# Optimization experiments

Measured on AMD Instinct MI355X. Metric: run time of the kernel, lower is better.

The kernel has to match this reference:

```python
import jax, jax.numpy as jnp
import numpy as np


def setup_inputs() -> dict:
    key = jax.random.key(0)
    k_u, k_a, k_b, k_c, k_d = jax.random.split(key, 5)
    B, T, Din, Dout, S = 16, 4096, 256, 256, 256
    return {
        "u": jax.random.normal(k_u, (B, T, Din), dtype=jnp.float32),
        "a_raw": jnp.zeros((S,), dtype=jnp.float32),
        "b": jax.random.normal(k_b, (S, Din), dtype=jnp.float32) * 0.1,
        "c": jax.random.normal(k_c, (Dout, S), dtype=jnp.float32) * 0.1,
        "d": jax.random.normal(k_d, (Dout, Din), dtype=jnp.float32) * 0.1,
    }


def reference(u, a_raw, b, c, d):
    # u: (B, T, Din) -> y: (B, T, Dout)
    # Recurrence: x_t = a * x_{t-1} + b @ u_t ;  y_t = c @ x_t + d @ u_t
    a = jnp.tanh(a_raw)                                  # (S,)
    Bu = jnp.einsum('btd,sd->bts', u, b)                 # input projection, (B,T,S)

    def step(x, bu_t):
        x = x * a + bu_t                                 # diagonal state update
        return x, x

    x0 = jnp.zeros((u.shape[0], a.shape[0]), dtype=u.dtype)
    _, xs = jax.lax.scan(step, x0, jnp.swapaxes(Bu, 0, 1))  # xs: (T,B,S)
    xs = jnp.swapaxes(xs, 0, 1)                              # (B,T,S)

    y = jnp.einsum('bts,os->bto', xs, c) + jnp.einsum('bti,oi->bto', u, d)
    return y  # dropout(p=0.0) is identity
```

## Files before the change

### kernel.cpp

```cpp
#include <hip/hip_runtime.h>

#define DEV __device__ __forceinline__

typedef unsigned short u16;
typedef __attribute__((ext_vector_type(8))) __bf16 bf16x8;
typedef __attribute__((ext_vector_type(4))) float f32x4;
typedef __attribute__((ext_vector_type(8))) unsigned short u16x8;

static constexpr int NCH_TOT = 1024;

DEV u16 f2bf(float f) {
  unsigned u = __builtin_bit_cast(unsigned, f);
  u += 0x7fffu + ((u >> 16) & 1u);
  return (u16)(u >> 16);
}
DEV float bf2f(u16 h) {
  unsigned u = ((unsigned)h) << 16;
  return __builtin_bit_cast(float, u);
}

DEV void gl_lds16(const void* gp, void* lp) {
  __builtin_amdgcn_global_load_lds(
      (__attribute__((address_space(1))) void*)(void*)gp,
      (__attribute__((address_space(3))) void*)lp, 16, 0, 0);
}

__global__ __launch_bounds__(256) void prep_k(const float* __restrict__ a_raw,
                                              const float* __restrict__ b,
                                              const float* __restrict__ c,
                                              const float* __restrict__ d,
                                              float* __restrict__ af,
                                              u16* __restrict__ bw,
                                              u16* __restrict__ cw,
                                              u16* __restrict__ dw) {
  int i = blockIdx.x * 256 + threadIdx.x;
  if (i < 256) af[i] = tanhf(a_raw[i]);
  bw[i] = f2bf(b[i]);
  cw[i] = f2bf(c[i]);
  dw[i] = f2bf(d[i]);
}

__global__ __launch_bounds__(256) void convu_k(const float* __restrict__ u,
                                               u16* __restrict__ ub) {
  size_t i = ((size_t)blockIdx.x * 256 + threadIdx.x) * 8;
  float4 v0 = *reinterpret_cast<const float4*>(u + i);
  float4 v1 = *reinterpret_cast<const float4*>(u + i + 4);
  u16x8 o;
  o[0] = f2bf(v0.x); o[1] = f2bf(v0.y); o[2] = f2bf(v0.z); o[3] = f2bf(v0.w);
  o[4] = f2bf(v1.x); o[5] = f2bf(v1.y); o[6] = f2bf(v1.z); o[7] = f2bf(v1.w);
  *reinterpret_cast<u16x8*>(ub + i) = o;
}

__global__ __launch_bounds__(256) void gemm1_k(const u16* __restrict__ ubf,
                                               const u16* __restrict__ bw,
                                               const float* __restrict__ af,
                                               u16* __restrict__ bu,
                                               float* __restrict__ carry4) {
  __shared__ u16 As[128 * 64];
  __shared__ u16 Bs[128 * 64];
  const int tid = threadIdx.x;
  const int lane = tid & 63;
  const int wid = tid >> 6;
  const int wm = wid >> 1, wn = wid & 1;
  const int panel = blockIdx.x;
  const size_t row0 = (size_t)blockIdx.y * 128;
  const int col0 = panel * 128;

  const int rstg = tid >> 3;
  const int c16 = tid & 7;

  const f32x4 zero = {0.f, 0.f, 0.f, 0.f};
  f32x4 acc[4][4];
#pragma unroll
  for (int i = 0; i < 4; ++i)
#pragma unroll
    for (int j = 0; j < 4; ++j) acc[i][j] = zero;

#pragma unroll
  for (int kt = 0; kt < 4; ++kt) {
    const int kb = kt * 64;
#pragma unroll
    for (int j = 0; j < 4; ++j) {
      int row = j * 32 + rstg;
      int sc = c16 ^ (row & 7);
      gl_lds16(ubf + (row0 + row) * 256 + kb + sc * 8,
               (char*)As + j * 4096 + wid * 1024);
      gl_lds16(bw + (size_t)(col0 + row) * 256 + kb + sc * 8,
               (char*)Bs + j * 4096 + wid * 1024);
    }
    __syncthreads();
#pragma unroll
    for (int kk = 0; kk < 2; ++kk) {
      const int ks = kk * 4 + (lane >> 4);
      bf16x8 afr[4], bfr[4];
#pragma unroll
      for (int mi = 0; mi < 4; ++mi) {
        int ar = wm * 64 + mi * 16 + (lane & 15);
        afr[mi] = *reinterpret_cast<const bf16x8*>(&As[ar * 64 + (ks ^ (ar & 7)) * 8]);
      }
#pragma unroll
      for (int ni = 0; ni < 4; ++ni) {
        int br = wn * 64 + ni * 16 + (lane & 15);
        bfr[ni] = *reinterpret_cast<const bf16x8*>(&Bs[br * 64 + (ks ^ (br & 7)) * 8]);
      }
#pragma unroll
      for (int mi = 0; mi < 4; ++mi)
#pragma unroll
        for (int ni = 0; ni < 4; ++ni)
          acc[mi][ni] = __builtin_amdgcn_mfma_f32_16x16x32_bf16(
              afr[mi], bfr[ni], acc[mi][ni], 0, 0, 0);
    }
    if (kt < 3) __syncthreads();
  }

  const size_t t2 = (size_t)blockIdx.y * 2 + wm;
#pragma unroll
  for (int mi = 0; mi < 4; ++mi) {
    int rbase = mi * 16 + (lane >> 4) * 4;
#pragma unroll
    for (int ni = 0; ni < 4; ++ni) {
      int col = col0 + wn * 64 + ni * 16 + (lane & 15);
      int colpart = (col >> 6) * 4096 + (col & 7);
      int sl = (col >> 3) & 7;
#pragma unroll
      for (int q = 0; q < 4; ++q) {
        int r = rbase + q;
        bu[t2 * 16384 + colpart + r * 64 + ((sl ^ (r & 7)) * 8)] = f2bf(acc[mi][ni][q]);
      }
    }
  }

  {
    const int tb = (lane >> 4) * 4;
#pragma unroll
    for (int ni = 0; ni < 4; ++ni) {
      int col = col0 + wn * 64 + ni * 16 + (lane & 15);
      float a = af[col];
      float c2 = a * a, c4 = c2 * c2, c8 = c4 * c4, a12 = c8 * c4;
      float base = (tb == 0) ? a12 : (tb == 4) ? c8 : (tb == 8) ? c4 : 1.0f;
#pragma unroll
      for (int mi = 0; mi < 4; ++mi) {
        float p = base, sq = 0.f;
#pragma unroll
        for (int q = 3; q >= 0; --q) {
          sq = fmaf(p, acc[mi][ni][q], sq);
          if (q) p *= a;
        }
        sq += __shfl_xor(sq, 16, 64);
        sq += __shfl_xor(sq, 32, 64);
        if ((lane >> 4) == 0) carry4[t2 * 1024 + mi * 256 + col] = sq;
      }
    }
  }
}

__global__ __launch_bounds__(256) void scan2_k(const float* __restrict__ carry4,
                                               const float* __restrict__ af,
                                               float* __restrict__ initb4) {
  int b = blockIdx.x;
  int s = threadIdx.x;
  float a = af[s];
  float a16 = a * a; a16 = a16 * a16; a16 = a16 * a16; a16 = a16 * a16;
  float x = 0.f;
  size_t base = (size_t)b * 64 * 1024 + s;
  float c0 = carry4[base], c1 = carry4[base + 256],
        c2 = carry4[base + 512], c3 = carry4[base + 768];
  for (int k = 0; k < 64; ++k) {
    size_t idx = base + (size_t)k * 1024;
    float n0 = 0.f, n1 = 0.f, n2 = 0.f, n3 = 0.f;
    if (k < 63) {
      size_t nx = idx + 1024;
      n0 = carry4[nx]; n1 = carry4[nx + 256]; n2 = carry4[nx + 512]; n3 = carry4[nx + 768];
    }
    initb4[idx] = x;        x = fmaf(a16, x, c0);
    initb4[idx + 256] = x;  x = fmaf(a16, x, c1);
    initb4[idx + 512] = x;  x = fmaf(a16, x, c2);
    initb4[idx + 768] = x;  x = fmaf(a16, x, c3);
    c0 = n0; c1 = n1; c2 = n2; c3 = n3;
  }
}

__global__ __launch_bounds__(512, 6) void gemm2_k(const u16* __restrict__ bu,
                                                  const u16* __restrict__ cw,
                                                  const u16* __restrict__ dw,
                                                  const u16* __restrict__ ubf,
                                                  const float* __restrict__ af,
                                                  const float* __restrict__ initb4,
                                                  float* __restrict__ y) {
  __shared__ u16 XS[64 * 256];
  __shared__ u16 CS[128 * 64];
  const int tid = threadIdx.x;
  const int lane = tid & 63;
  const int wid = tid >> 6;
  const int wr = wid >> 2, wc = wid & 3;
  const int by = blockIdx.y;
  const int col0 = blockIdx.x * 128;

  const char* src = (const char*)bu + (size_t)by * 32768;
#pragma unroll
  for (int j = 0; j < 4; ++j)
    gl_lds16(src + j * 8192 + tid * 16, (char*)XS + j * 8192 + wid * 1024);
#pragma unroll
  for (int rr = 0; rr < 2; ++rr) {
    int brow = rr * 64 + (tid >> 3);
    int sc = (tid & 7) ^ (brow & 7);
    gl_lds16(cw + (size_t)(col0 + brow) * 256 + sc * 8,
             (char*)CS + rr * 8192 + wid * 1024);
  }
  __syncthreads();

  {
    const int s = tid & 255;
    const int pair = tid >> 8;
    const float a = af[s];
    const int colpart = (s >> 6) * 4096 + (s & 7);
    const int sl = (s >> 3) & 7;
    float x1 = initb4[(size_t)by * 1024 + (pair * 2) * 256 + s];
    float x2 = initb4[(size_t)by * 1024 + (pair * 2 + 1) * 256 + s];
    const int rA0 = pair * 32, rB0 = pair * 32 + 16;
    float vA[16], vB[16];
#pragma unroll
    for (int t = 0; t < 16; ++t) {
      int rA = rA0 + t, rB = rB0 + t;
      vA[t] = bf2f(XS[colpart + rA * 64 + ((sl ^ (rA & 7)) * 8)]);
      vB[t] = bf2f(XS[colpart + rB * 64 + ((sl ^ (rB & 7)) * 8)]);
    }
#pragma unroll
    for (int t = 0; t < 16; ++t) {
      x1 = fmaf(a, x1, vA[t]); vA[t] = x1;
      x2 = fmaf(a, x2, vB[t]); vB[t] = x2;
    }
#pragma unroll
    for (int t = 0; t < 16; ++t) {
      int rA = rA0 + t, rB = rB0 + t;
      XS[colpart + rA * 64 + ((sl ^ (rA & 7)) * 8)] = f2bf(vA[t]);
      XS[colpart + rB * 64 + ((sl ^ (rB & 7)) * 8)] = f2bf(vB[t]);
    }
  }
  __syncthreads();

  f32x4 acc[2][2];
  const f32x4 zero = {0.f, 0.f, 0.f, 0.f};
  acc[0][0] = zero; acc[0][1] = zero; acc[1][0] = zero; acc[1][1] = zero;

#pragma unroll
  for (int kt8 = 0; kt8 < 8; ++kt8) {
#pragma unroll
    for (int kk = 0; kk < 2; ++kk) {
      const int ksl = kk * 4 + (lane >> 4);
      bf16x8 afr[2], bfr[2];
#pragma unroll
      for (int mi = 0; mi < 2; ++mi) {
        int ar = wr * 32 + mi * 16 + (lane & 15);
        afr[mi] = *reinterpret_cast<const bf16x8*>(
            &XS[(kt8 & 3) * 4096 + ar * 64 + ((ksl ^ (ar & 7)) * 8)]);
      }
#pragma unroll
      for (int ni = 0; ni < 2; ++ni) {
        int nr = wc * 32 + ni * 16 + (lane & 15);
        bfr[ni] = *reinterpret_cast<const bf16x8*>(&CS[nr * 64 + ((ksl ^ (nr & 7)) * 8)]);
      }
#pragma unroll
      for (int mi = 0; mi < 2; ++mi)
#pragma unroll
        for (int ni = 0; ni < 2; ++ni)
          acc[mi][ni] = __builtin_amdgcn_mfma_f32_16x16x32_bf16(
              afr[mi], bfr[ni], acc[mi][ni], 0, 0, 0);
    }
    if (kt8 < 7) {
      __syncthreads();
      if (kt8 < 4) {
        int r = tid >> 3, cs = tid & 7;
        gl_lds16(ubf + ((size_t)by * 64 + r) * 256 + kt8 * 64 + ((cs ^ (r & 7)) * 8),
                 (char*)XS + kt8 * 8192 + wid * 1024);
      }
      const u16* Wn = (kt8 < 3) ? cw : dw;
      const int kb = (kt8 < 3) ? (kt8 + 1) * 64 : (kt8 - 3) * 64;
#pragma unroll
      for (int rr = 0; rr < 2; ++rr) {
        int brow = rr * 64 + (tid >> 3);
        int sc = (tid & 7) ^ (brow & 7);
        gl_lds16(Wn + (size_t)(col0 + brow) * 256 + kb + sc * 8,
                 (char*)CS + rr * 8192 + wid * 1024);
      }
      __syncthreads();
    }
  }

#pragma unroll
  for (int mi = 0; mi < 2; ++mi) {
    int rlb = wr * 32 + mi * 16 + (lane >> 4) * 4;
#pragma unroll
    for (int ni = 0; ni < 2; ++ni) {
      int col = col0 + wc * 32 + ni * 16 + (lane & 15);
#pragma unroll
      for (int q = 0; q < 4; ++q)
        y[((size_t)by * 64 + rlb + q) * 256 + col] = acc[mi][ni][q];
    }
  }
}

extern "C" void kernel_launch(void* const* d_in, const int* in_sizes, int n_in,
                              void* d_out, int out_size, void* d_ws, size_t ws_size,
                              hipStream_t stream) {
  const float* u = (const float*)d_in[0];
  const float* a_raw = (const float*)d_in[1];
  const float* b = (const float*)d_in[2];
  const float* c = (const float*)d_in[3];
  const float* d = (const float*)d_in[4];
  float* y = (float*)d_out;
  char* ws = (char*)d_ws;

  const size_t MB = 1u << 20;
  float* af = (float*)(ws);
  u16* bw = (u16*)(ws + 4096);
  u16* cw = (u16*)(ws + 4096 + 131072);
  u16* dw = (u16*)(ws + 4096 + 2 * 131072);
  u16* ubf = (u16*)(ws + 1 * MB);
  u16* bu = (u16*)(ws + 33 * MB);
  float* carry4 = (float*)(ws + 65 * MB);
  float* initb4 = (float*)(ws + 69 * MB);

  prep_k<<<256, 256, 0, stream>>>(a_raw, b, c, d, af, bw, cw, dw);
  convu_k<<<8192, 256, 0, stream>>>(u, ubf);
  gemm1_k<<<dim3(2, 512), 256, 0, stream>>>(ubf, bw, af, bu, carry4);
  scan2_k<<<16, 256, 0, stream>>>(carry4, af, initb4);
  gemm2_k<<<dim3(2, 1024), 512, 0, stream>>>(bu, cw, dw, ubf, af, initb4, y);
}
```

Measured before the change: 96.27 us.

## Double-buffer LDS tiles in both GEMM kernels to overlap loads with MFMA

gemm1 and gemm2 now keep two LDS buffers for the weight/input tiles. Each k-step issues the next tile's async global-to-LDS loads before running the MFMAs on the current tile, which removes one barrier per step and hides load latency behind compute. gemm2 also prefetches the second C tile during the in-LDS scan, and splits that scan into 8-step segments to cut register pressure. The costs are more LDS per block, a lower launch-bounds occupancy hint (6 to 4), and one redundant reload of C tile 1 on the first iteration.

After: 100.5 us. 1.04x slower.

```diff
diff --git a/kernel.cpp b/kernel.cpp
--- a/kernel.cpp
+++ b/kernel.cpp
@@ -6,8 +6,6 @@
 typedef __attribute__((ext_vector_type(8))) __bf16 bf16x8;
 typedef __attribute__((ext_vector_type(4))) float f32x4;
 typedef __attribute__((ext_vector_type(8))) unsigned short u16x8;
-
-static constexpr int NCH_TOT = 1024;
 
 DEV u16 f2bf(float f) {
   unsigned u = __builtin_bit_cast(unsigned, f);
@@ -56,8 +54,8 @@
                                                const float* __restrict__ af,
                                                u16* __restrict__ bu,
                                                float* __restrict__ carry4) {
-  __shared__ u16 As[128 * 64];
-  __shared__ u16 Bs[128 * 64];
+  __shared__ u16 As[2 * 128 * 64];
+  __shared__ u16 Bs[2 * 128 * 64];
   const int tid = threadIdx.x;
   const int lane = tid & 63;
   const int wid = tid >> 6;
@@ -76,19 +74,28 @@
 #pragma unroll
     for (int j = 0; j < 4; ++j) acc[i][j] = zero;
 
+#define G1_STAGE(ktv, bufv)                                                  \
+  {                                                                          \
+    const int kb_ = (ktv) * 64;                                              \
+    _Pragma("unroll") for (int j = 0; j < 4; ++j) {                          \
+      int row = j * 32 + rstg;                                               \
+      int sc = c16 ^ (row & 7);                                              \
+      gl_lds16(ubf + (row0 + row) * 256 + kb_ + sc * 8,                      \
+               (char*)As + (bufv)*16384 + j * 4096 + wid * 1024);            \
+      gl_lds16(bw + (size_t)(col0 + row) * 256 + kb_ + sc * 8,               \
+               (char*)Bs + (bufv)*16384 + j * 4096 + wid * 1024);            \
+    }                                                                        \
+  }
+
+  G1_STAGE(0, 0);
+  __syncthreads();
+
 #pragma unroll
   for (int kt = 0; kt < 4; ++kt) {
-    const int kb = kt * 64;
-#pragma unroll
-    for (int j = 0; j < 4; ++j) {
-      int row = j * 32 + rstg;
-      int sc = c16 ^ (row & 7);
-      gl_lds16(ubf + (row0 + row) * 256 + kb + sc * 8,
-               (char*)As + j * 4096 + wid * 1024);
-      gl_lds16(bw + (size_t)(col0 + row) * 256 + kb + sc * 8,
-               (char*)Bs + j * 4096 + wid * 1024);
-    }
-    __syncthreads();
+    const int cur = kt & 1;
+    if (kt < 3) G1_STAGE(kt + 1, cur ^ 1);
+    const u16* Ab = As + cur * 8192;
+    const u16* Bb = Bs + cur * 8192;
 #pragma unroll
     for (int kk = 0; kk < 2; ++kk) {
       const int ks = kk * 4 + (lane >> 4);
@@ -96,12 +103,12 @@
 #pragma unroll
       for (int mi = 0; mi < 4; ++mi) {
         int ar = wm * 64 + mi * 16 + (lane & 15);
-        afr[mi] = *reinterpret_cast<const bf16x8*>(&As[ar * 64 + (ks ^ (ar & 7)) * 8]);
+        afr[mi] = *reinterpret_cast<const bf16x8*>(&Ab[ar * 64 + (ks ^ (ar & 7)) * 8]);
       }
 #pragma unroll
       for (int ni = 0; ni < 4; ++ni) {
         int br = wn * 64 + ni * 16 + (lane & 15);
-        bfr[ni] = *reinterpret_cast<const bf16x8*>(&Bs[br * 64 + (ks ^ (br & 7)) * 8]);
+        bfr[ni] = *reinterpret_cast<const bf16x8*>(&Bb[br * 64 + (ks ^ (br & 7)) * 8]);
       }
 #pragma unroll
       for (int mi = 0; mi < 4; ++mi)
@@ -180,7 +187,7 @@
   }
 }
 
-__global__ __launch_bounds__(512, 6) void gemm2_k(const u16* __restrict__ bu,
+__global__ __launch_bounds__(512, 4) void gemm2_k(const u16* __restrict__ bu,
                                                   const u16* __restrict__ cw,
                                                   const u16* __restrict__ dw,
                                                   const u16* __restrict__ ubf,
@@ -188,7 +195,7 @@
                                                   const float* __restrict__ initb4,
                                                   float* __restrict__ y) {
   __shared__ u16 XS[64 * 256];
-  __shared__ u16 CS[128 * 64];
+  __shared__ u16 CS[2 * 128 * 64];
   const int tid = threadIdx.x;
   const int lane = tid & 63;
   const int wid = tid >> 6;
@@ -196,18 +203,24 @@
   const int by = blockIdx.y;
   const int col0 = blockIdx.x * 128;
 
+#define G2_CS_STAGE(Wp, kbv, bufv)                                           \
+  {                                                                          \
+    _Pragma("unroll") for (int rr = 0; rr < 2; ++rr) {                       \
+      int brow = rr * 64 + (tid >> 3);                                       \
+      int sc = (tid & 7) ^ (brow & 7);                                       \
+      gl_lds16((Wp) + (size_t)(col0 + brow) * 256 + (kbv) + sc * 8,          \
+               (char*)CS + (bufv)*16384 + rr * 8192 + wid * 1024);           \
+    }                                                                        \
+  }
+
   const char* src = (const char*)bu + (size_t)by * 32768;
 #pragma unroll
   for (int j = 0; j < 4; ++j)
     gl_lds16(src + j * 8192 + tid * 16, (char*)XS + j * 8192 + wid * 1024);
-#pragma unroll
-  for (int rr = 0; rr < 2; ++rr) {
-    int brow = rr * 64 + (tid >> 3);
-    int sc = (tid & 7) ^ (brow & 7);
-    gl_lds16(cw + (size_t)(col0 + brow) * 256 + sc * 8,
-             (char*)CS + rr * 8192 + wid * 1024);
-  }
+  G2_CS_STAGE(cw, 0, 0);
   __syncthreads();
+
+  G2_CS_STAGE(cw, 64, 1);
 
   {
     const int s = tid & 255;
@@ -217,25 +230,26 @@
     const int sl = (s >> 3) & 7;
     float x1 = initb4[(size_t)by * 1024 + (pair * 2) * 256 + s];
     float x2 = initb4[(size_t)by * 1024 + (pair * 2 + 1) * 256 + s];
-    const int rA0 = pair * 32, rB0 = pair * 32 + 16;
-    float vA[16], vB[16];
-#pragma unroll
-    for (int t = 0; t < 16; ++t) {
-      int rA = rA0 + t, rB = rB0 + t;
-      vA[t] = bf2f(XS[colpart + rA * 64 + ((sl ^ (rA & 7)) * 8)]);
-      vB[t] = bf2f(XS[colpart + rB * 64 + ((sl ^ (rB & 7)) * 8)]);
-    }
-#pragma unroll
-    for (int t = 0; t < 16; ++t) {
-      x1 = fmaf(a, x1, vA[t]); vA[t] = x1;
-      x2 = fmaf(a, x2, vB[t]); vB[t] = x2;
-    }
-#pragma unroll
-    for (int t = 0; t < 16; ++t) {
-      int rA = rA0 + t, rB = rB0 + t;
-      XS[colpart + rA * 64 + ((sl ^ (rA & 7)) * 8)] = f2bf(vA[t]);
-      XS[colpart + rB * 64 + ((sl ^ (rB & 7)) * 8)] = f2bf(vB[t]);
-    }
+#define SEG(xv, rb0)                                                          \
+  {                                                                           \
+    float v[8];                                                               \
+    _Pragma("unroll") for (int t = 0; t < 8; ++t) {                           \
+      int r = (rb0) + t;                                                      \
+      v[t] = bf2f(XS[colpart + r * 64 + ((sl ^ (r & 7)) * 8)]);               \
+    }                                                                         \
+    _Pragma("unroll") for (int t = 0; t < 8; ++t) {                           \
+      xv = fmaf(a, xv, v[t]); v[t] = xv;                                      \
+    }                                                                         \
+    _Pragma("unroll") for (int t = 0; t < 8; ++t) {                           \
+      int r = (rb0) + t;                                                      \
+      XS[colpart + r * 64 + ((sl ^ (r & 7)) * 8)] = f2bf(v[t]);               \
+    }                                                                         \
+  }
+    SEG(x1, pair * 32 + 0);
+    SEG(x1, pair * 32 + 8);
+    SEG(x2, pair * 32 + 16);
+    SEG(x2, pair * 32 + 24);
+#undef SEG
   }
   __syncthreads();
 
@@ -245,6 +259,18 @@
 
 #pragma unroll
   for (int kt8 = 0; kt8 < 8; ++kt8) {
+    if (kt8 >= 1 && kt8 <= 4) {
+      int qq = kt8 - 1;
+      int r = tid >> 3, cs = tid & 7;
+      gl_lds16(ubf + ((size_t)by * 64 + r) * 256 + qq * 64 + ((cs ^ (r & 7)) * 8),
+               (char*)XS + qq * 8192 + wid * 1024);
+    }
+    if (kt8 < 7) {
+      if (kt8 + 1 < 4) G2_CS_STAGE(cw, (kt8 + 1) * 64, (kt8 + 1) & 1)
+      else             G2_CS_STAGE(dw, (kt8 - 3) * 64, (kt8 + 1) & 1)
+    }
+    const u16* CSb = CS + (kt8 & 1) * 8192;
+    const u16* XSq = XS + (kt8 & 3) * 4096;
 #pragma unroll
     for (int kk = 0; kk < 2; ++kk) {
       const int ksl = kk * 4 + (lane >> 4);
@@ -252,13 +278,12 @@
 #pragma unroll
       for (int mi = 0; mi < 2; ++mi) {
         int ar = wr * 32 + mi * 16 + (lane & 15);
-        afr[mi] = *reinterpret_cast<const bf16x8*>(
-            &XS[(kt8 & 3) * 4096 + ar * 64 + ((ksl ^ (ar & 7)) * 8)]);
+        afr[mi] = *reinterpret_cast<const bf16x8*>(&XSq[ar * 64 + ((ksl ^ (ar & 7)) * 8)]);
       }
 #pragma unroll
       for (int ni = 0; ni < 2; ++ni) {
         int nr = wc * 32 + ni * 16 + (lane & 15);
-        bfr[ni] = *reinterpret_cast<const bf16x8*>(&CS[nr * 64 + ((ksl ^ (nr & 7)) * 8)]);
+        bfr[ni] = *reinterpret_cast<const bf16x8*>(&CSb[nr * 64 + ((ksl ^ (nr & 7)) * 8)]);
       }
 #pragma unroll
       for (int mi = 0; mi < 2; ++mi)
@@ -267,24 +292,7 @@
           acc[mi][ni] = __builtin_amdgcn_mfma_f32_16x16x32_bf16(
               afr[mi], bfr[ni], acc[mi][ni], 0, 0, 0);
     }
-    if (kt8 < 7) {
-      __syncthreads();
-      if (kt8 < 4) {
-        int r = tid >> 3, cs = tid & 7;
-        gl_lds16(ubf + ((size_t)by * 64 + r) * 256 + kt8 * 64 + ((cs ^ (r & 7)) * 8),
-                 (char*)XS + kt8 * 8192 + wid * 1024);
-      }
-      const u16* Wn = (kt8 < 3) ? cw : dw;
-      const int kb = (kt8 < 3) ? (kt8 + 1) * 64 : (kt8 - 3) * 64;
-#pragma unroll
-      for (int rr = 0; rr < 2; ++rr) {
-        int brow = rr * 64 + (tid >> 3);
-        int sc = (tid & 7) ^ (brow & 7);
-        gl_lds16(Wn + (size_t)(col0 + brow) * 256 + kb + sc * 8,
-                 (char*)CS + rr * 8192 + wid * 1024);
-      }
-      __syncthreads();
-    }
+    if (kt8 < 7) __syncthreads();
   }
 
 #pragma unroll
```
